# Kernel tuning notes

Measured on AMD Instinct MI355X. Metric: run time of the kernel, lower is better.

## Reference

```python
import jax, jax.numpy as jnp
import numpy as np

# args of SimilarityLoss
B, N_WAY, N_SHOT, QUERY, NUM_SLOT, H = 128, 5, 1, 15, 32, 256
LAMBDA = 1.0


def setup_inputs() -> dict:
    key = jax.random.key(0)
    k1, k2, k3, k4 = jax.random.split(key, 4)
    out_f = jax.random.normal(k1, (B * N_WAY * (N_SHOT + QUERY), NUM_SLOT, H), jnp.float32)
    labels_support = jax.random.randint(k2, (B, N_WAY * N_SHOT), 0, N_WAY)  # unused by forward
    labels_query = jax.random.randint(k3, (B, QUERY, N_WAY, 1), 0, N_WAY)
    att_loss = jax.random.uniform(k4, (), jnp.float32)
    return {"out_f": out_f, "labels_support": labels_support,
            "labels_query": labels_query, "att_loss": att_loss, "mode": 0}


def _max_select(scores):
    # scores: [b, n_way, num_slot]. Greedy unique top-1 slot per class, classes in order.
    b, n_way, num_slot = scores.shape
    order = jnp.argsort(-scores, axis=-1)  # descending sort indices per class row
    used = jnp.zeros((b, num_slot), dtype=bool)
    rows = jnp.arange(b)
    sel = []
    for j in range(n_way):  # tiny fixed loop over classes (sequential dependency)
        row = order[:, j, :]                       # [b, num_slot]
        avail = ~used[rows[:, None], row]          # [b, num_slot]
        pos = jnp.argmax(avail, axis=1)            # first unused slot position
        pick = row[rows, pos]                      # [b]
        used = used.at[rows, pick].set(True)
        sel.append(pick)
    return jnp.stack(sel, axis=1)                  # [b, n_way]


def _normalize(x):
    # F.normalize(p=2, eps=1e-12) semantics
    n = jnp.linalg.norm(x, axis=-1, keepdims=True)
    return x / jnp.maximum(n, 1e-12)


def _forward(out_f, labels_query, att_loss):
    b = labels_query.shape[0]
    ns = b * N_WAY * N_SHOT
    sup = out_f[:ns].reshape(b, N_WAY, N_SHOT, NUM_SLOT, H).mean(axis=2)   # [b, n_way, num_slot, H]
    qry = out_f[ns:].reshape(b, N_WAY, QUERY, NUM_SLOT, H)

    sel = _max_select(sup.mean(-1))                                        # [b, n_way]

    idx_s = jnp.broadcast_to(sel[:, None, :, None], (b, N_WAY, N_WAY, H))
    sup_sel = jnp.take_along_axis(sup, idx_s, axis=2)                      # [b, n_way, n_way, H]
    idx_q = jnp.broadcast_to(sel[:, None, None, :, None], (b, N_WAY, QUERY, N_WAY, H))
    qry_sel = jnp.take_along_axis(qry, idx_q, axis=3).reshape(b, N_WAY * QUERY, N_WAY, H)

    sn = _normalize(sup_sel)
    qn = _normalize(qry_sel)

    diag = jnp.arange(N_WAY)
    proto = sn[:, diag, diag, :]                                           # support[i, j, j] -> [b, n_way, H]
    diff = jnp.sum((qn - proto[:, None, :, :]) ** 2, axis=-1)              # [b, n_way*query, n_way]

    # NB: raw-memory reshape (n_way, query) -> (query, n_way) exactly as the torch code does
    logits = jax.nn.log_softmax(-diff, axis=2).reshape(b, QUERY, N_WAY, N_WAY)

    nll = -jnp.take_along_axis(logits, labels_query, axis=3)               # [b, query, n_way, 1]
    loss = nll.mean() + jnp.float32(LAMBDA) * att_loss

    y_hat = jnp.argmax(logits, axis=3)                                     # [b, query, n_way]
    acc = jnp.mean((y_hat == labels_query[..., 0]).astype(jnp.float32))
    return loss, acc


def reference(out_f, labels_support, labels_query, att_loss, mode):
    return _forward(out_f, labels_query, att_loss)
```

## Files before the change

kernel.cpp:

```cpp
#include <hip/hip_runtime.h>

#define B_       128
#define N_WAY    5
#define QUERY    15
#define NUM_SLOT 32
#define H_       256
#define NS       (B_ * N_WAY)
#define NQ       (B_ * N_WAY * QUERY)
#define ROW      (NUM_SLOT * H_)
#define SPB      (N_WAY * QUERY)
#define RPB      (N_WAY * NUM_SLOT)
#define NBLK_MAIN (NQ / 4)

__device__ __forceinline__ float wave_reduce(float v) {
    for (int m = 32; m > 0; m >>= 1) v += __shfl_xor(v, m, 64);
    return v;
}

__global__ __launch_bounds__(1024)
void k_batch(const float* __restrict__ out_f, int* __restrict__ sel,
             float* __restrict__ proto) {
    int b = blockIdx.x;
    int t = threadIdx.x, wid = t >> 6, lane = t & 63;
    __shared__ float sc[RPB];
    __shared__ int ssel[N_WAY];

    const float* base = out_f + (size_t)b * RPB * H_;
    for (int i = wid; i < RPB; i += 32) {
        float4 v0 = ((const float4*)(base + (size_t)i * H_))[lane];
        float4 v1 = ((const float4*)(base + (size_t)(i + 16) * H_))[lane];
        float s0 = wave_reduce(v0.x + v0.y + v0.z + v0.w);
        float s1 = wave_reduce(v1.x + v1.y + v1.z + v1.w);
        if (lane == 0) { sc[i] = s0 * (1.0f / H_); sc[i + 16] = s1 * (1.0f / H_); }
    }
    __syncthreads();

    if (t == 0) {
        unsigned used = 0u;
        for (int j = 0; j < N_WAY; ++j) {
            float best = -INFINITY; int bi = 0;
            #pragma unroll
            for (int s = 0; s < NUM_SLOT; ++s) {
                bool ok = !((used >> s) & 1u);
                float v = sc[j * NUM_SLOT + s];
                if (ok && v > best) { best = v; bi = s; }
            }
            used |= 1u << bi;
            ssel[j] = bi;
        }
        #pragma unroll
        for (int j = 0; j < N_WAY; ++j) sel[b * N_WAY + j] = ssel[j];
    }
    __syncthreads();

    if (wid < N_WAY) {
        int k = wid;
        int r = b * N_WAY + k;
        const float4* p = (const float4*)(base + ((size_t)k * NUM_SLOT + ssel[k]) * H_);
        float4 v = p[lane];
        float s2 = wave_reduce(v.x*v.x + v.y*v.y + v.z*v.z + v.w*v.w);
        float inv = 1.0f / fmaxf(sqrtf(s2), 1e-12f);
        ((float4*)(proto + (size_t)r * H_))[lane] =
            make_float4(v.x*inv, v.y*inv, v.z*inv, v.w*inv);
    }
}

__global__ __launch_bounds__(256)
void k_main(const float* __restrict__ out_f, const int* __restrict__ sel,
            const float* __restrict__ proto, const int* __restrict__ labels_q,
            float2* __restrict__ part) {
    int wid = threadIdx.x >> 6, lane = threadIdx.x & 63;
    int id = blockIdx.x * 4 + wid;
    int b = id / SPB;
    const float* qrow = out_f + (size_t)(NS + id) * ROW;

    float diffs[N_WAY];
    #pragma unroll
    for (int k = 0; k < N_WAY; ++k) {
        int slot = sel[b * N_WAY + k];
        float4 qv = ((const float4*)(qrow + (size_t)slot * H_))[lane];
        float4 pv = ((const float4*)(proto + (size_t)(b * N_WAY + k) * H_))[lane];
        float s2 = qv.x*qv.x + qv.y*qv.y + qv.z*qv.z + qv.w*qv.w;
        float dt = qv.x*pv.x + qv.y*pv.y + qv.z*pv.z + qv.w*pv.w;
        float p2 = pv.x*pv.x + pv.y*pv.y + pv.z*pv.z + pv.w*pv.w;
        for (int m = 32; m > 0; m >>= 1) {
            s2 += __shfl_xor(s2, m, 64);
            dt += __shfl_xor(dt, m, 64);
            p2 += __shfl_xor(p2, m, 64);
        }
        float inv = 1.0f / fmaxf(sqrtf(s2), 1e-12f);
        diffs[k] = s2 * inv * inv - 2.0f * dt * inv + p2;
    }

    __shared__ float s_n[4], s_c[4];
    if (lane == 0) {
        int l = labels_q[id];
        float mn = diffs[0]; int am = 0;
        #pragma unroll
        for (int k = 1; k < N_WAY; ++k)
            if (diffs[k] < mn) { mn = diffs[k]; am = k; }
        float se = 0.0f;
        #pragma unroll
        for (int k = 0; k < N_WAY; ++k) se += expf(mn - diffs[k]);
        s_n[wid] = diffs[l] - mn + logf(se);
        s_c[wid] = (am == l) ? 1.0f : 0.0f;
    }
    __syncthreads();
    if (threadIdx.x == 0)
        part[blockIdx.x] = make_float2(s_n[0] + s_n[1] + s_n[2] + s_n[3],
                                       s_c[0] + s_c[1] + s_c[2] + s_c[3]);
}

__global__ __launch_bounds__(256)
void k_finalize(const float2* __restrict__ part, const float* __restrict__ att_loss,
                float* __restrict__ out) {
    __shared__ float sa[4], sb[4];
    int t = threadIdx.x, wid = t >> 6, lane = t & 63;
    float a = 0.0f, c = 0.0f;
    for (int i = t; i < NBLK_MAIN; i += 256) { float2 p = part[i]; a += p.x; c += p.y; }
    a = wave_reduce(a); c = wave_reduce(c);
    if (lane == 0) { sa[wid] = a; sb[wid] = c; }
    __syncthreads();
    if (t == 0) {
        float sn_ = sa[0] + sa[1] + sa[2] + sa[3];
        float sc_ = sb[0] + sb[1] + sb[2] + sb[3];
        out[0] = sn_ * (1.0f / NQ) + att_loss[0];
        out[1] = sc_ * (1.0f / NQ);
    }
}

extern "C" void kernel_launch(void* const* d_in, const int* in_sizes, int n_in,
                              void* d_out, int out_size, void* d_ws, size_t ws_size,
                              hipStream_t stream) {
    const float* out_f    = (const float*)d_in[0];
    const int*   labels_q = (const int*)d_in[2];
    const float* att_loss = (const float*)d_in[3];
    float* out = (float*)d_out;

    float*  ws    = (float*)d_ws;
    int*    sel   = (int*)ws;
    float*  proto = ws + 640;
    float2* part  = (float2*)(ws + 640 + 163840);

    k_batch   <<<B_,        1024, 0, stream>>>(out_f, sel, proto);
    k_main    <<<NBLK_MAIN, 256,  0, stream>>>(out_f, sel, proto, labels_q, part);
    k_finalize<<<1,         256,  0, stream>>>(part, att_loss, out);
}
```

Before: 34.22 us.

## Fuse slot selection, prototype normalization and query scoring into one kernel

Merges the per-batch selection kernel and the per-query scoring kernel into one kernel of 256 blocks, two per batch, each splitting that batch's 75 queries. Prototypes and their squared norms stay in shared memory rather than passing through global workspace. This removes one launch and the workspace round-trip. Each half-block redundantly recomputes the 160-row slot mean scan and the greedy selection, and the grid becomes much smaller, with far fewer waves in flight for the gathered query loads.

```diff
diff --git a/kernel.cpp b/kernel.cpp
--- a/kernel.cpp
+++ b/kernel.cpp
@@ -10,7 +10,7 @@
 #define ROW      (NUM_SLOT * H_)
 #define SPB      (N_WAY * QUERY)
 #define RPB      (N_WAY * NUM_SLOT)
-#define NBLK_MAIN (NQ / 4)
+#define NBLK     (2 * B_)
 
 __device__ __forceinline__ float wave_reduce(float v) {
     for (int m = 32; m > 0; m >>= 1) v += __shfl_xor(v, m, 64);
@@ -18,12 +18,16 @@
 }
 
 __global__ __launch_bounds__(1024)
-void k_batch(const float* __restrict__ out_f, int* __restrict__ sel,
-             float* __restrict__ proto) {
-    int b = blockIdx.x;
+void k_fused(const float* __restrict__ out_f, const int* __restrict__ labels_q,
+             float2* __restrict__ part) {
+    int blk = blockIdx.x, b = blk >> 1, half = blk & 1;
     int t = threadIdx.x, wid = t >> 6, lane = t & 63;
+
     __shared__ float sc[RPB];
     __shared__ int ssel[N_WAY];
+    __shared__ __align__(16) float pl[N_WAY][H_];
+    __shared__ float p2s[N_WAY];
+    __shared__ float s_n[16], s_c[16];
 
     const float* base = out_f + (size_t)b * RPB * H_;
     for (int i = wid; i < RPB; i += 32) {
@@ -48,67 +52,66 @@
             used |= 1u << bi;
             ssel[j] = bi;
         }
-        #pragma unroll
-        for (int j = 0; j < N_WAY; ++j) sel[b * N_WAY + j] = ssel[j];
     }
     __syncthreads();
 
     if (wid < N_WAY) {
         int k = wid;
-        int r = b * N_WAY + k;
-        const float4* p = (const float4*)(base + ((size_t)k * NUM_SLOT + ssel[k]) * H_);
-        float4 v = p[lane];
+        float4 v = ((const float4*)(base + ((size_t)k * NUM_SLOT + ssel[k]) * H_))[lane];
         float s2 = wave_reduce(v.x*v.x + v.y*v.y + v.z*v.z + v.w*v.w);
         float inv = 1.0f / fmaxf(sqrtf(s2), 1e-12f);
-        ((float4*)(proto + (size_t)r * H_))[lane] =
-            make_float4(v.x*inv, v.y*inv, v.z*inv, v.w*inv);
-    }
-}
-
-__global__ __launch_bounds__(256)
-void k_main(const float* __restrict__ out_f, const int* __restrict__ sel,
-            const float* __restrict__ proto, const int* __restrict__ labels_q,
-            float2* __restrict__ part) {
-    int wid = threadIdx.x >> 6, lane = threadIdx.x & 63;
-    int id = blockIdx.x * 4 + wid;
-    int b = id / SPB;
-    const float* qrow = out_f + (size_t)(NS + id) * ROW;
-
-    float diffs[N_WAY];
-    #pragma unroll
-    for (int k = 0; k < N_WAY; ++k) {
-        int slot = sel[b * N_WAY + k];
-        float4 qv = ((const float4*)(qrow + (size_t)slot * H_))[lane];
-        float4 pv = ((const float4*)(proto + (size_t)(b * N_WAY + k) * H_))[lane];
-        float s2 = qv.x*qv.x + qv.y*qv.y + qv.z*qv.z + qv.w*qv.w;
-        float dt = qv.x*pv.x + qv.y*pv.y + qv.z*pv.z + qv.w*pv.w;
-        float p2 = pv.x*pv.x + pv.y*pv.y + pv.z*pv.z + pv.w*pv.w;
-        for (int m = 32; m > 0; m >>= 1) {
-            s2 += __shfl_xor(s2, m, 64);
-            dt += __shfl_xor(dt, m, 64);
-            p2 += __shfl_xor(p2, m, 64);
-        }
-        float inv = 1.0f / fmaxf(sqrtf(s2), 1e-12f);
-        diffs[k] = s2 * inv * inv - 2.0f * dt * inv + p2;
-    }
-
-    __shared__ float s_n[4], s_c[4];
-    if (lane == 0) {
-        int l = labels_q[id];
-        float mn = diffs[0]; int am = 0;
-        #pragma unroll
-        for (int k = 1; k < N_WAY; ++k)
-            if (diffs[k] < mn) { mn = diffs[k]; am = k; }
-        float se = 0.0f;
-        #pragma unroll
-        for (int k = 0; k < N_WAY; ++k) se += expf(mn - diffs[k]);
-        s_n[wid] = diffs[l] - mn + logf(se);
-        s_c[wid] = (am == l) ? 1.0f : 0.0f;
+        float4 nv = make_float4(v.x*inv, v.y*inv, v.z*inv, v.w*inv);
+        *(float4*)&pl[k][lane * 4] = nv;
+        float p2 = wave_reduce(nv.x*nv.x + nv.y*nv.y + nv.z*nv.z + nv.w*nv.w);
+        if (lane == 0) p2s[k] = p2;
     }
     __syncthreads();
-    if (threadIdx.x == 0)
-        part[blockIdx.x] = make_float2(s_n[0] + s_n[1] + s_n[2] + s_n[3],
-                                       s_c[0] + s_c[1] + s_c[2] + s_c[3]);
+
+    int sBeg = half ? 38 : 0;
+    int sEnd = half ? SPB : 38;
+    float accn = 0.0f, accc = 0.0f;
+    for (int s = sBeg + wid; s < sEnd; s += 16) {
+        int id = b * SPB + s;
+        const float* qrow = out_f + (size_t)(NS + id) * ROW;
+        float4 qv[N_WAY];
+        #pragma unroll
+        for (int k = 0; k < N_WAY; ++k)
+            qv[k] = ((const float4*)(qrow + (size_t)ssel[k] * H_))[lane];
+        float diffs[N_WAY];
+        #pragma unroll
+        for (int k = 0; k < N_WAY; ++k) {
+            float4 pv = *(const float4*)&pl[k][lane * 4];
+            float s2 = qv[k].x*qv[k].x + qv[k].y*qv[k].y + qv[k].z*qv[k].z + qv[k].w*qv[k].w;
+            float dt = qv[k].x*pv.x + qv[k].y*pv.y + qv[k].z*pv.z + qv[k].w*pv.w;
+            for (int m = 32; m > 0; m >>= 1) {
+                s2 += __shfl_xor(s2, m, 64);
+                dt += __shfl_xor(dt, m, 64);
+            }
+            float inv = 1.0f / fmaxf(sqrtf(s2), 1e-12f);
+            diffs[k] = s2 * inv * inv - 2.0f * dt * inv + p2s[k];
+        }
+        if (lane == 0) {
+            int l = labels_q[id];
+            float mn = diffs[0]; int am = 0;
+            #pragma unroll
+            for (int k = 1; k < N_WAY; ++k)
+                if (diffs[k] < mn) { mn = diffs[k]; am = k; }
+            float se = 0.0f;
+            #pragma unroll
+            for (int k = 0; k < N_WAY; ++k) se += expf(mn - diffs[k]);
+            accn += diffs[l] - mn + logf(se);
+            accc += (am == l) ? 1.0f : 0.0f;
+        }
+    }
+    if (lane == 0) { s_n[wid] = accn; s_c[wid] = accc; }
+    __syncthreads();
+
+    if (t == 0) {
+        float a = 0.0f, c = 0.0f;
+        #pragma unroll
+        for (int i = 0; i < 16; ++i) { a += s_n[i]; c += s_c[i]; }
+        part[blk] = make_float2(a, c);
+    }
 }
 
 __global__ __launch_bounds__(256)
@@ -116,9 +119,9 @@
                 float* __restrict__ out) {
     __shared__ float sa[4], sb[4];
     int t = threadIdx.x, wid = t >> 6, lane = t & 63;
-    float a = 0.0f, c = 0.0f;
-    for (int i = t; i < NBLK_MAIN; i += 256) { float2 p = part[i]; a += p.x; c += p.y; }
-    a = wave_reduce(a); c = wave_reduce(c);
+    float2 p = part[t];
+    float a = wave_reduce(p.x);
+    float c = wave_reduce(p.y);
     if (lane == 0) { sa[wid] = a; sb[wid] = c; }
     __syncthreads();
     if (t == 0) {
@@ -137,12 +140,8 @@
     const float* att_loss = (const float*)d_in[3];
     float* out = (float*)d_out;
 
-    float*  ws    = (float*)d_ws;
-    int*    sel   = (int*)ws;
-    float*  proto = ws + 640;
-    float2* part  = (float2*)(ws + 640 + 163840);
+    float2* part = (float2*)d_ws;
 
-    k_batch   <<<B_,        1024, 0, stream>>>(out_f, sel, proto);
-    k_main    <<<NBLK_MAIN, 256,  0, stream>>>(out_f, sel, proto, labels_q, part);
-    k_finalize<<<1,         256,  0, stream>>>(part, att_loss, out);
+    k_fused   <<<NBLK, 1024, 0, stream>>>(out_f, labels_q, part);
+    k_finalize<<<1,    256,  0, stream>>>(part, att_loss, out);
 }
```

New measurement: 30.08 us. 12.1% less time.
